# Performance work log

Hardware: AMD Instinct MI355X
Metric: run time of the kernel (lower is better)

Reference implementation:

```python
import jax, jax.numpy as jnp
import numpy as np

BATCH = 8192
IN_DIM = 512
OUT_DIM = 512
GRID_SIZE = 5
SPLINE_ORDER = 3
# grid has 2*(G+K)+1 knots -> after K de Boor steps basis count = 2*G+K
N_BASES = 2 * GRID_SIZE + SPLINE_ORDER  # 13
CLAMP_EPS = 1e-4
DENOM_EPS = 1e-8


def _make_grid():
    step = 2.0 / GRID_SIZE
    g = jnp.arange(-GRID_SIZE - SPLINE_ORDER, GRID_SIZE + SPLINE_ORDER + 1, dtype=jnp.float32) * step
    return jnp.tile(g[None, :], (IN_DIM, 1))  # [in_dim, 2*(G+K)+1]


def _b_spline(x, grid):
    # x: [B, in], grid: [in, L] -> bases: [B, in, 2*G+K]
    xg = x[..., None]  # [B, in, 1]
    bases = ((xg >= grid[:, :-1]) & (xg < grid[:, 1:])).astype(x.dtype)
    for k in range(1, SPLINE_ORDER + 1):
        denom1 = grid[:, k:-1] - grid[:, :-(k + 1)] + DENOM_EPS
        left = (xg - grid[:, :-(k + 1)]) / denom1
        denom2 = grid[:, k + 1:] - grid[:, 1:-k] + DENOM_EPS
        right = (grid[:, k + 1:] - xg) / denom2
        bases = left * bases[..., :-1] + right * bases[..., 1:]
    return bases


def setup_inputs() -> dict:
    key = jax.random.key(0)
    k1, k2, k3 = jax.random.split(key, 3)
    x = jax.random.normal(k1, (BATCH, IN_DIM), dtype=jnp.float32)
    # kaiming_uniform(a=sqrt(5)) ~ U(-1/sqrt(fan_in), 1/sqrt(fan_in))
    b_c = 1.0 / np.sqrt(IN_DIM * N_BASES)
    coeffs = jax.random.uniform(k2, (OUT_DIM, IN_DIM, N_BASES), dtype=jnp.float32, minval=-b_c, maxval=b_c)
    b_w = 1.0 / np.sqrt(IN_DIM)
    base_weight = jax.random.uniform(k3, (OUT_DIM, IN_DIM), dtype=jnp.float32, minval=-b_w, maxval=b_w)
    return {"x": x, "coeffs": coeffs, "base_weight": base_weight}


def reference(x, coeffs, base_weight):
    grid = _make_grid()
    xc = jnp.clip(x, -1.0 + CLAMP_EPS, 1.0 - CLAMP_EPS)
    basis = _b_spline(xc, grid)                       # [B, in, nb]
    spline_out = jnp.einsum('oic,bic->bo', coeffs, basis)
    base_out = jax.nn.silu(x) @ base_weight.T         # F.linear(silu(x), W)
    y = spline_out + base_out + x                     # residual (in_dim == out_dim)
    return y
```

## Files before the change

kernel.cpp:

```cpp
#include <hip/hip_runtime.h>
#include <stdint.h>

typedef unsigned int u32;
typedef unsigned short u16;
typedef unsigned long long u64;
typedef __bf16 bf16x8 __attribute__((ext_vector_type(8)));
typedef float f32x4 __attribute__((ext_vector_type(4)));
typedef u32 u32x4 __attribute__((ext_vector_type(4)));

#define IN_DIM 512

__device__ __forceinline__ u16 bfr(float f) {
  __bf16 h = (__bf16)f;
  return __builtin_bit_cast(u16, h);
}
__device__ __forceinline__ u16 f2bf(float f) {
  u32 u = __builtin_bit_cast(u32, f);
  u += 0x7fffu + ((u >> 16) & 1u);
  return (u16)(u >> 16);
}
__device__ __forceinline__ u32 pk2(float a, float b) {
  return (u32)f2bf(a) | ((u32)f2bf(b) << 16);
}

__global__ void pack_b(const float* __restrict__ coeffs,
                       const float* __restrict__ bw,
                       char* __restrict__ Bp) {
  __shared__ float stage[64][56];
  const int tid = threadIdx.x;
  const int q = tid & 3, g = tid >> 2;
  const int id = blockIdx.x * 64 + g;
  const int col = id >> 7, s = id & 127;
  const float* cbase = coeffs + ((size_t)col * IN_DIM + s * 4) * 13;
#pragma unroll
  for (int j = 0; j < 3; ++j) {
    int ch = q + j * 4;
    float4 v = *(const float4*)(cbase + ch * 4);
    stage[g][ch * 4 + 0] = v.x; stage[g][ch * 4 + 1] = v.y;
    stage[g][ch * 4 + 2] = v.z; stage[g][ch * 4 + 3] = v.w;
  }
  if (q == 0) {
    float4 v = *(const float4*)(cbase + 48);
    stage[g][48] = v.x; stage[g][49] = v.y; stage[g][50] = v.z; stage[g][51] = v.w;
  }
  if (q == 1) {
    float4 v = *(const float4*)(bw + (size_t)col * IN_DIM + s * 4);
    stage[g][52] = v.x; stage[g][53] = v.y; stage[g][54] = v.z; stage[g][55] = v.w;
  }
  __syncthreads();
  const int nbp = col >> 7, cb = (col >> 4) & 7, cl = col & 15;
  char* base = Bp + (((size_t)(nbp * 128 + s) * 8 + cb) * 2) * 1024;
#pragma unroll
  for (int r = 0; r < 2; ++r) {
    int idx = q * 2 + r;
    int h = idx & 1;
    int dd = idx >> 1;
    int ks = dd >> 1;
    const float* sf = &stage[g][dd * 13];
    float w = stage[g][52 + dd];
    u16 hh[8];
#pragma unroll
    for (int c = 0; c < 8; ++c) {
      int slot = h * 8 + c;
      float v = slot < 13 ? sf[slot] : (slot < 15 ? w : 0.0f);
      hh[c] = bfr(v);
    }
    u32x4 o;
    o.x = (u32)hh[0] | ((u32)hh[1] << 16);
    o.y = (u32)hh[2] | ((u32)hh[3] << 16);
    o.z = (u32)hh[4] | ((u32)hh[5] << 16);
    o.w = (u32)hh[6] | ((u32)hh[7] << 16);
    int lanei = cl + 16 * (2 * (dd & 1) + h);
    *(u32x4*)(base + (size_t)ks * 1024 + lanei * 16) = o;
  }
}

__device__ __forceinline__ void expandA(float xv, char* rb, u32 swz, u32 k0) {
  float xc = fminf(fmaxf(xv, -0.9999f), 0.9999f);
  float tp = __fmaf_rn(xc, 2.5f, 3.0f);
  float fj = floorf(tp);
  int jl = (int)fj;
  float u = tp - fj;
  float u2 = u * u, u3 = u2 * u;
  float vv = 1.0f - u;
  float b0 = vv * vv * vv * (1.0f / 6.0f);
  float b3 = u3 * (1.0f / 6.0f);
  float b1 = __fmaf_rn(0.5f, u3, __fmaf_rn(u2, -1.0f, 2.0f / 3.0f));
  float b2 = 1.0f - b0 - b1 - b3;
  float e = __expf(-xv);
  float sg = __fdividef(xv, 1.0f + e);
  u16 sh = bfr(sg);
  float shf = __builtin_bit_cast(float, ((u32)sh) << 16);
  u16 sl = bfr(sg - shf);
  u32 pk01 = (u32)bfr(b0) | ((u32)bfr(b1) << 16);
  u32 pk23 = (u32)bfr(b2) | ((u32)bfr(b3) << 16);
  u64 v = (u64)pk01 | (((u64)pk23) << 32);
  int sstart = jl + 2;
  int qa = sstart >> 2;
  int shn = (sstart & 3) << 4;
  u64 lo = v << shn;
  u64 hi = shn ? (v >> (64 - shn)) : 0ull;
  u64 q0 = qa ? 0ull : lo;
  u64 q1 = qa ? lo : hi;
  u64 q2 = qa ? hi : 0ull;
  u64 q3 = (u64)(((u32)sh) << 16) | (((u64)(u32)sl) << 32);
  u32x4 c0, c1;
  c0.x = (u32)q0; c0.y = (u32)(q0 >> 32); c0.z = (u32)q1; c0.w = (u32)(q1 >> 32);
  c1.x = (u32)q2; c1.y = (u32)(q2 >> 32); c1.z = (u32)q3; c1.w = (u32)(q3 >> 32);
  *(u32x4*)(rb + ((k0 ^ swz) << 4)) = c0;
  *(u32x4*)(rb + (((k0 + 1u) ^ swz) << 4)) = c1;
}

__launch_bounds__(512, 2)
__global__ void kan_gemm(const float* __restrict__ x,
                         const char* __restrict__ Bp,
                         float* __restrict__ out) {
  __shared__ __align__(16) char smem[128 * 129 * 4];

  const int tid = threadIdx.x;
  const int lane = tid & 63;
  const int wid = tid >> 6;
  const int kt = wid >> 2;
  const int wm = (wid >> 1) & 1, wn = wid & 1;
  const int lrow = lane & 15, lkg = lane >> 4;

  int s0 = blockIdx.x;
  int xcd = s0 & 7;
  int nb = xcd >> 1;
  int mb = ((s0 >> 3) << 1) | (xcd & 1);

  const int arow = tid >> 2, ad = tid & 3;
  const u32 aswz = (u32)(arow & 7);
  const u32 ak0 = (u32)(ad * 2);
  const float* xp = x + (size_t)(mb * 128 + arow) * IN_DIM + ad;

  const char* bptr = Bp + (((size_t)(nb * 128) * 8 + wn * 4) * 2 + kt) * 1024 + (size_t)lane * 16;

  f32x4 acc[4][4];
#pragma unroll
  for (int i = 0; i < 4; ++i)
#pragma unroll
    for (int j = 0; j < 4; ++j) acc[i][j] = (f32x4){0.f, 0.f, 0.f, 0.f};

  u32x4 bA[4], bB[4];
  expandA(xp[0], smem + arow * 128, aswz, ak0);
#pragma unroll
  for (int fn = 0; fn < 4; ++fn)
    bA[fn] = *(const u32x4*)(bptr + fn * 2048);
  float xn1 = xp[4];
  float xn2 = xp[8];
  __syncthreads();

  const char* arb_base = smem + (wm * 64 + lrow) * 128;
  const u32 asl = (((u32)(kt * 4) | (u32)lkg) ^ (u32)(lrow & 7)) << 4;

#define GEMM_STEP(SN, NXT_OFF, CUR_OFF, BCUR, BNXT)                            \
  {                                                                            \
      \
    bf16x8 af[4];                                                              \
    _Pragma("unroll")                                                          \
    for (int fm = 0; fm < 4; ++fm)                                             \
      af[fm] = __builtin_bit_cast(bf16x8,                                      \
          *(const u32x4*)(arb_base + (CUR_OFF) + fm * 2048 + asl));            \
     \
    int sl_ = (SN) < 128 ? (SN) : 127;                                         \
    _Pragma("unroll")                                                          \
    for (int fn = 0; fn < 4; ++fn)                                             \
      BNXT[fn] = *(const u32x4*)(bptr + (size_t)sl_ * 16384 + fn * 2048);      \
    float xload = xp[((SN) + 2 < 128 ? (SN) + 2 : 127) * 4];                   \
                                  \
    if ((SN) < 128) expandA(xn1, smem + (NXT_OFF) + arow * 128, aswz, ak0);    \
    xn1 = xn2; xn2 = xload;                                                    \
                                                  \
    __builtin_amdgcn_s_setprio(1);                                             \
    _Pragma("unroll")                                                          \
    for (int fm = 0; fm < 4; ++fm)                                             \
      _Pragma("unroll")                                                        \
      for (int fn = 0; fn < 4; ++fn)                                           \
        acc[fm][fn] = __builtin_amdgcn_mfma_f32_16x16x32_bf16(                 \
            af[fm], __builtin_bit_cast(bf16x8, BCUR[fn]), acc[fm][fn], 0, 0, 0);\
    __builtin_amdgcn_s_setprio(0);                                             \
     \
    asm volatile("s_waitcnt lgkmcnt(0)" ::: "memory");                         \
    __builtin_amdgcn_s_barrier();                                              \
  }

#pragma unroll 1
  for (int s = 0; s < 128; s += 2) {
    GEMM_STEP(s + 1, 16384, 0, bA, bB)
    GEMM_STEP(s + 2, 0, 16384, bB, bA)
  }

  __syncthreads();

  float* red = (float*)smem;
  if (kt == 1) {
#pragma unroll
    for (int fm = 0; fm < 4; ++fm)
#pragma unroll
      for (int fn = 0; fn < 4; ++fn) {
        int rr = wm * 64 + fm * 16 + lkg * 4;
        int cc = wn * 64 + fn * 16 + lrow;
#pragma unroll
        for (int r = 0; r < 4; ++r)
          red[(size_t)(rr + r) * 129 + cc] = acc[fm][fn][r];
      }
  }
  __syncthreads();
  if (kt == 0) {
#pragma unroll
    for (int fm = 0; fm < 4; ++fm)
#pragma unroll
      for (int fn = 0; fn < 4; ++fn) {
        int rr = wm * 64 + fm * 16 + lkg * 4;
        int cc = wn * 64 + fn * 16 + lrow;
        size_t gb = (size_t)(mb * 128 + rr) * IN_DIM + nb * 128 + cc;
#pragma unroll
        for (int r = 0; r < 4; ++r) {
          size_t off = gb + (size_t)r * IN_DIM;
          out[off] = acc[fm][fn][r] + red[(size_t)(rr + r) * 129 + cc] + x[off];
        }
      }
  }
}

__device__ __forceinline__ void st_b16(char* rb, u32 swz, u32 k0, int c, u16 v) {
  u32 uc = (u32)c;
  u32 byte = (((k0 + (uc >> 3)) ^ swz) << 4) | ((uc & 7u) << 1);
  *(u16*)(rb + byte) = v;
}

__device__ __forceinline__ void stage_a_fb(char* aT, int row, int d, float xv) {
  char* rb = aT + row * 128;
  u32 swz = (u32)(row & 7);
  float xc = fminf(fmaxf(xv, -0.9999f), 0.9999f);
  float tp = __fmaf_rn(xc, 2.5f, 3.0f);
  float fj = floorf(tp);
  int jl = (int)fj;
  float u = tp - fj;
  float u2 = u * u, u3 = u2 * u;
  float vv = 1.0f - u;
  float b0 = vv * vv * vv * (1.0f / 6.0f);
  float b3 = u3 * (1.0f / 6.0f);
  float b1 = __fmaf_rn(0.5f, u3, __fmaf_rn(u2, -1.0f, 2.0f / 3.0f));
  float b2 = 1.0f - b0 - b1 - b3;
  float e = __expf(-xv);
  float sg = __fdividef(xv, 1.0f + e);
  u16 sh = f2bf(sg);
  float shf = __builtin_bit_cast(float, ((u32)sh) << 16);
  u16 slo = f2bf(sg - shf);
  u32 k0 = (u32)d * 2u;
  u32x4 z = {0u, 0u, 0u, 0u};
  *(u32x4*)(rb + ((k0 ^ swz) << 4)) = z;
  u32x4 z2 = {0u, 0u, ((u32)sh) << 16, (u32)slo};
  *(u32x4*)(rb + (((k0 + 1u) ^ swz) << 4)) = z2;
  st_b16(rb, swz, k0, jl + 2, f2bf(b0));
  st_b16(rb, swz, k0, jl + 3, f2bf(b1));
  st_b16(rb, swz, k0, jl + 4, f2bf(b2));
  st_b16(rb, swz, k0, jl + 5, f2bf(b3));
}

__launch_bounds__(512, 2)
__global__ void kan_fused(const float* __restrict__ x,
                          const float* __restrict__ coeffs,
                          const float* __restrict__ bw,
                          float* __restrict__ out) {
  __shared__ __align__(16) char smem[65536];
  const int tid = threadIdx.x;
  const int lane = tid & 63;
  const int wid = tid >> 6;
  const int team = wid >> 2;
  const int wm = (wid >> 1) & 1;
  const int wn = wid & 1;
  const int m0 = wm * 64, n0 = wn * 64;
  const int lrow = lane & 15;
  const int lkg = lane >> 4;
  int s = blockIdx.x;
  int xcd = s & 7;
  int nb = xcd >> 1;
  int mb = (s >> 3) | ((xcd & 1) << 5);
  const int t = tid & 255;
  const int arow = t >> 1;
  const int h = t & 1;
  char* aT = smem + team * 16384;
  char* bT = smem + 32768 + team * 16384;
  const int dim0 = team * 256;
  const float* xptr = x + (size_t)(mb * 128 + arow) * IN_DIM + dim0 + 2 * h;
  const float* cptr = coeffs + ((size_t)((nb * 128 + arow) * IN_DIM) + dim0) * 13 + 26 * h;
  const float* wptr = bw + (size_t)(nb * 128 + arow) * IN_DIM + dim0 + 2 * h;
  f32x4 acc[4][4];
#pragma unroll
  for (int i = 0; i < 4; ++i)
#pragma unroll
    for (int j = 0; j < 4; ++j) acc[i][j] = (f32x4){0.f, 0.f, 0.f, 0.f};
  float2 xv, wv;
  float2 cv0, cv1, cv2, cv3, cv4, cv5, cv6, cv7, cv8, cv9, cv10, cv11, cv12;
#define PREFETCH(STP)                                                     \
  {                                                                       \
    const float* cp_ = cptr + (STP) * 52;                                 \
    xv = *(const float2*)(xptr + (STP) * 4);                              \
    wv = *(const float2*)(wptr + (STP) * 4);                              \
    cv0 = *(const float2*)(cp_ + 0);   cv1 = *(const float2*)(cp_ + 2);   \
    cv2 = *(const float2*)(cp_ + 4);   cv3 = *(const float2*)(cp_ + 6);   \
    cv4 = *(const float2*)(cp_ + 8);   cv5 = *(const float2*)(cp_ + 10);  \
    cv6 = *(const float2*)(cp_ + 12);  cv7 = *(const float2*)(cp_ + 14);  \
    cv8 = *(const float2*)(cp_ + 16);  cv9 = *(const float2*)(cp_ + 18);  \
    cv10 = *(const float2*)(cp_ + 20); cv11 = *(const float2*)(cp_ + 22); \
    cv12 = *(const float2*)(cp_ + 24);                                    \
  }
  PREFETCH(0)
  for (int st = 0; st < 64; ++st) {
    stage_a_fb(aT, arow, 2 * h + 0, xv.x);
    stage_a_fb(aT, arow, 2 * h + 1, xv.y);
    {
      char* rb = bT + arow * 128;
      u32 swz = (u32)(arow & 7);
      u32 k0 = (u32)(2 * h) * 2u;
      u32x4 lo, hi;
      lo.x = pk2(cv0.x, cv0.y); lo.y = pk2(cv1.x, cv1.y);
      lo.z = pk2(cv2.x, cv2.y); lo.w = pk2(cv3.x, cv3.y);
      hi.x = pk2(cv4.x, cv4.y); hi.y = pk2(cv5.x, cv5.y);
      {
        u16 wb = f2bf(wv.x);
        hi.z = (u32)f2bf(cv6.x) | ((u32)wb << 16);
        hi.w = (u32)wb;
      }
      *(u32x4*)(rb + ((k0 ^ swz) << 4)) = lo;
      *(u32x4*)(rb + (((k0 + 1u) ^ swz) << 4)) = hi;
      lo.x = pk2(cv6.y, cv7.x);  lo.y = pk2(cv7.y, cv8.x);
      lo.z = pk2(cv8.y, cv9.x);  lo.w = pk2(cv9.y, cv10.x);
      hi.x = pk2(cv10.y, cv11.x); hi.y = pk2(cv11.y, cv12.x);
      {
        u16 wb = f2bf(wv.y);
        hi.z = (u32)f2bf(cv12.y) | ((u32)wb << 16);
        hi.w = (u32)wb;
      }
      *(u32x4*)(rb + (((k0 + 2u) ^ swz) << 4)) = lo;
      *(u32x4*)(rb + (((k0 + 3u) ^ swz) << 4)) = hi;
    }
    __syncthreads();
    if (st != 63) { PREFETCH(st + 1) }
    {
      const char* arb = aT + (m0 + lrow) * 128;
      const char* brb = bT + (n0 + lrow) * 128;
      u32 rsw = (u32)(lrow & 7);
#pragma unroll
      for (int ks = 0; ks < 2; ++ks) {
        u32 sl2 = (((u32)(ks * 4) | (u32)lkg) ^ rsw) << 4;
        bf16x8 af[4], bfr2[4];
#pragma unroll
        for (int fm = 0; fm < 4; ++fm)
          af[fm] = __builtin_bit_cast(bf16x8, *(const u32x4*)(arb + fm * 2048 + sl2));
#pragma unroll
        for (int fn = 0; fn < 4; ++fn)
          bfr2[fn] = __builtin_bit_cast(bf16x8, *(const u32x4*)(brb + fn * 2048 + sl2));
#pragma unroll
        for (int fm = 0; fm < 4; ++fm)
#pragma unroll
          for (int fn = 0; fn < 4; ++fn)
            acc[fm][fn] = __builtin_amdgcn_mfma_f32_16x16x32_bf16(
                af[fm], bfr2[fn], acc[fm][fn], 0, 0, 0);
      }
    }
    __syncthreads();
  }
  float* red = (float*)smem;
  if (team == 1) {
#pragma unroll
    for (int fm = 0; fm < 4; ++fm)
#pragma unroll
      for (int fn = 0; fn < 4; ++fn) {
        int rr = m0 + fm * 16 + lkg * 4;
        int cc = n0 + fn * 16 + lrow;
#pragma unroll
        for (int r = 0; r < 4; ++r) red[(rr + r) * 128 + cc] = acc[fm][fn][r];
      }
  }
  __syncthreads();
  if (team == 0) {
#pragma unroll
    for (int fm = 0; fm < 4; ++fm)
#pragma unroll
      for (int fn = 0; fn < 4; ++fn) {
        int rr = m0 + fm * 16 + lkg * 4;
        int ccol = n0 + fn * 16 + lrow;
        int grow = mb * 128 + rr;
        int gcol = nb * 128 + ccol;
#pragma unroll
        for (int r = 0; r < 4; ++r) {
          float v = acc[fm][fn][r] + red[(rr + r) * 128 + ccol] +
                    x[(size_t)(grow + r) * IN_DIM + gcol];
          out[(size_t)(grow + r) * IN_DIM + gcol] = v;
        }
      }
  }
}

extern "C" void kernel_launch(void* const* d_in, const int* in_sizes, int n_in,
                              void* d_out, int out_size, void* d_ws, size_t ws_size,
                              hipStream_t stream) {
  const float* x = (const float*)d_in[0];
  const float* coeffs = (const float*)d_in[1];
  const float* bw = (const float*)d_in[2];
  float* out = (float*)d_out;
  if (ws_size >= (size_t)512 * 16384) {
    char* Bp = (char*)d_ws;
    hipLaunchKernelGGL(pack_b, dim3(1024), dim3(256), 0, stream, coeffs, bw, Bp);
    hipLaunchKernelGGL(kan_gemm, dim3(256), dim3(512), 0, stream, x, Bp, out);
  } else {
    hipLaunchKernelGGL(kan_fused, dim3(256), dim3(512), 0, stream, x, coeffs, bw, out);
  }
}
```

Measured before the change: 98.11 us.

## Warp-specialize GEMM: dedicated producer waves expand A into triple-buffered LDS

The block grows from 8 to 12 waves. Eight consumer waves only load B and issue MFMAs, while four producer waves compute the B-spline expansion of x into a rotating triple buffer in shared memory, working two steps ahead. The goal is to take the ALU-heavy basis expansion off the MFMA waves' critical path so it overlaps with matrix work. In exchange the block is larger, the launch bound becomes 768 threads with 3 blocks per SM, shared memory grows, and the reduction stride changes from 129 to 132.

```diff
diff --git a/kernel.cpp b/kernel.cpp
--- a/kernel.cpp
+++ b/kernel.cpp
@@ -111,15 +111,17 @@
   *(u32x4*)(rb + (((k0 + 1u) ^ swz) << 4)) = c1;
 }
 
-__launch_bounds__(512, 2)
+__launch_bounds__(768, 3)
 __global__ void kan_gemm(const float* __restrict__ x,
                          const char* __restrict__ Bp,
                          float* __restrict__ out) {
-  __shared__ __align__(16) char smem[128 * 129 * 4];
+  __shared__ __align__(16) char smem[67584];
 
   const int tid = threadIdx.x;
   const int lane = tid & 63;
   const int wid = tid >> 6;
+  const bool isC = (wid < 8);
+
   const int kt = wid >> 2;
   const int wm = (wid >> 1) & 1, wn = wid & 1;
   const int lrow = lane & 15, lkg = lane >> 4;
@@ -129,10 +131,13 @@
   int nb = xcd >> 1;
   int mb = ((s0 >> 3) << 1) | (xcd & 1);
 
-  const int arow = tid >> 2, ad = tid & 3;
-  const u32 aswz = (u32)(arow & 7);
+  const int te = tid & 255;
+  const int erow = te >> 2;
+  const int ad = te & 3;
+  const u32 aswz = (u32)(erow & 7);
   const u32 ak0 = (u32)(ad * 2);
-  const float* xp = x + (size_t)(mb * 128 + arow) * IN_DIM + ad;
+  const float* xpa = x + (size_t)(mb * 128 + erow) * IN_DIM + ad;
+  const float* xpb = xpa + (size_t)64 * IN_DIM;
 
   const char* bptr = Bp + (((size_t)(nb * 128) * 8 + wn * 4) * 2 + kt) * 1024 + (size_t)lane * 16;
 
@@ -143,58 +148,73 @@
     for (int j = 0; j < 4; ++j) acc[i][j] = (f32x4){0.f, 0.f, 0.f, 0.f};
 
   u32x4 bA[4], bB[4];
-  expandA(xp[0], smem + arow * 128, aswz, ak0);
-#pragma unroll
-  for (int fn = 0; fn < 4; ++fn)
-    bA[fn] = *(const u32x4*)(bptr + fn * 2048);
-  float xn1 = xp[4];
-  float xn2 = xp[8];
+  char* r0 = smem;
+  char* r1 = smem + 16384;
+  char* r2 = smem + 32768;
+
+  float xa1 = 0.f, xa2 = 0.f, xb1 = 0.f, xb2 = 0.f;
+  if (isC) {
+#pragma unroll
+    for (int fn = 0; fn < 4; ++fn)
+      bA[fn] = *(const u32x4*)(bptr + fn * 2048);
+  } else {
+    expandA(xpa[0], r0 + erow * 128, aswz, ak0);
+    expandA(xpb[0], r0 + (erow + 64) * 128, aswz, ak0);
+    expandA(xpa[4], r1 + erow * 128, aswz, ak0);
+    expandA(xpb[4], r1 + (erow + 64) * 128, aswz, ak0);
+    xa1 = xpa[8];  xb1 = xpb[8];
+    xa2 = xpa[12]; xb2 = xpb[12];
+  }
   __syncthreads();
 
-  const char* arb_base = smem + (wm * 64 + lrow) * 128;
   const u32 asl = (((u32)(kt * 4) | (u32)lkg) ^ (u32)(lrow & 7)) << 4;
 
-#define GEMM_STEP(SN, NXT_OFF, CUR_OFF, BCUR, BNXT)                            \
+#define STEP(S, RB, WB, BCUR, BNXT)                                            \
   {                                                                            \
-      \
-    bf16x8 af[4];                                                              \
-    _Pragma("unroll")                                                          \
-    for (int fm = 0; fm < 4; ++fm)                                             \
-      af[fm] = __builtin_bit_cast(bf16x8,                                      \
-          *(const u32x4*)(arb_base + (CUR_OFF) + fm * 2048 + asl));            \
-     \
-    int sl_ = (SN) < 128 ? (SN) : 127;                                         \
-    _Pragma("unroll")                                                          \
-    for (int fn = 0; fn < 4; ++fn)                                             \
-      BNXT[fn] = *(const u32x4*)(bptr + (size_t)sl_ * 16384 + fn * 2048);      \
-    float xload = xp[((SN) + 2 < 128 ? (SN) + 2 : 127) * 4];                   \
-                                  \
-    if ((SN) < 128) expandA(xn1, smem + (NXT_OFF) + arow * 128, aswz, ak0);    \
-    xn1 = xn2; xn2 = xload;                                                    \
-                                                  \
-    __builtin_amdgcn_s_setprio(1);                                             \
-    _Pragma("unroll")                                                          \
-    for (int fm = 0; fm < 4; ++fm)                                             \
+    if (isC) {                                                                 \
+      bf16x8 af[4];                                                            \
+      const char* arb = (RB) + (wm * 64 + lrow) * 128;                         \
+      _Pragma("unroll")                                                        \
+      for (int fm = 0; fm < 4; ++fm)                                           \
+        af[fm] = __builtin_bit_cast(bf16x8,                                    \
+            *(const u32x4*)(arb + fm * 2048 + asl));                           \
+      int sl_ = (S) + 1 < 128 ? (S) + 1 : 127;                                 \
       _Pragma("unroll")                                                        \
       for (int fn = 0; fn < 4; ++fn)                                           \
-        acc[fm][fn] = __builtin_amdgcn_mfma_f32_16x16x32_bf16(                 \
-            af[fm], __builtin_bit_cast(bf16x8, BCUR[fn]), acc[fm][fn], 0, 0, 0);\
-    __builtin_amdgcn_s_setprio(0);                                             \
-     \
-    asm volatile("s_waitcnt lgkmcnt(0)" ::: "memory");                         \
+        BNXT[fn] = *(const u32x4*)(bptr + (size_t)sl_ * 16384 + fn * 2048);    \
+      __builtin_amdgcn_s_setprio(1);                                           \
+      _Pragma("unroll")                                                        \
+      for (int fm = 0; fm < 4; ++fm)                                           \
+        _Pragma("unroll")                                                      \
+        for (int fn = 0; fn < 4; ++fn)                                         \
+          acc[fm][fn] = __builtin_amdgcn_mfma_f32_16x16x32_bf16(               \
+              af[fm], __builtin_bit_cast(bf16x8, BCUR[fn]), acc[fm][fn],       \
+              0, 0, 0);                                                        \
+      __builtin_amdgcn_s_setprio(0);                                           \
+    } else {                                                                   \
+      if ((S) + 2 < 128) {                                                     \
+        expandA(xa1, (WB) + erow * 128, aswz, ak0);                            \
+        expandA(xb1, (WB) + (erow + 64) * 128, aswz, ak0);                     \
+      }                                                                        \
+      int xi = ((S) + 4 < 128 ? (S) + 4 : 127) * 4;                            \
+      float na = xpa[xi], nbv = xpb[xi];                                       \
+      xa1 = xa2; xa2 = na; xb1 = xb2; xb2 = nbv;                               \
+      asm volatile("s_waitcnt lgkmcnt(0)" ::: "memory");                       \
+    }                                                                          \
     __builtin_amdgcn_s_barrier();                                              \
   }
 
 #pragma unroll 1
   for (int s = 0; s < 128; s += 2) {
-    GEMM_STEP(s + 1, 16384, 0, bA, bB)
-    GEMM_STEP(s + 2, 0, 16384, bB, bA)
+    STEP(s, r0, r2, bA, bB)
+    STEP(s + 1, r1, r0, bB, bA)
+    char* t = r2; r2 = r1; r1 = r0; r0 = t;
   }
 
   __syncthreads();
 
   float* red = (float*)smem;
-  if (kt == 1) {
+  if (isC && kt == 1) {
 #pragma unroll
     for (int fm = 0; fm < 4; ++fm)
 #pragma unroll
@@ -203,11 +223,11 @@
         int cc = wn * 64 + fn * 16 + lrow;
 #pragma unroll
         for (int r = 0; r < 4; ++r)
-          red[(size_t)(rr + r) * 129 + cc] = acc[fm][fn][r];
+          red[(size_t)(rr + r) * 132 + cc] = acc[fm][fn][r];
       }
   }
   __syncthreads();
-  if (kt == 0) {
+  if (isC && kt == 0) {
 #pragma unroll
     for (int fm = 0; fm < 4; ++fm)
 #pragma unroll
@@ -218,7 +238,7 @@
 #pragma unroll
         for (int r = 0; r < 4; ++r) {
           size_t off = gb + (size_t)r * IN_DIM;
-          out[off] = acc[fm][fn][r] + red[(size_t)(rr + r) * 129 + cc] + x[off];
+          out[off] = acc[fm][fn][r] + red[(size_t)(rr + r) * 132 + cc] + x[off];
         }
       }
   }
@@ -406,7 +426,7 @@
   if (ws_size >= (size_t)512 * 16384) {
     char* Bp = (char*)d_ws;
     hipLaunchKernelGGL(pack_b, dim3(1024), dim3(256), 0, stream, coeffs, bw, Bp);
-    hipLaunchKernelGGL(kan_gemm, dim3(256), dim3(512), 0, stream, x, Bp, out);
+    hipLaunchKernelGGL(kan_gemm, dim3(256), dim3(768), 0, stream, x, Bp, out);
   } else {
     hipLaunchKernelGGL(kan_fused, dim3(256), dim3(512), 0, stream, x, coeffs, bw, out);
   }
```

After: 99.69 us. About the same (+1.6%).
